# Performance work log

Measured on AMD Instinct MI355X. Metric: run time of the kernel, lower is better.

Reference implementation:

```python
import jax, jax.numpy as jnp
import numpy as np

DIM = 2048
HIDDEN = 2048
HEADS = 4
HD = HIDDEN // HEADS  # head_dim = 512
EPS = 1e-6
BATCH = 4
SEQ = 2048


def setup_inputs() -> dict:
    key = jax.random.key(0)
    k0, k1, k2, k3 = jax.random.split(key, 4)
    s = 0.02  # typical init scale; keeps exp() input gate well-behaved
    x = jax.random.normal(k0, (BATCH, SEQ, DIM), dtype=jnp.float32)
    W_in = (jax.random.normal(k1, (HIDDEN, DIM), dtype=jnp.float32) * s)
    W_gate = (jax.random.normal(k2, (4 * HIDDEN, HIDDEN), dtype=jnp.float32) * s)
    b_gate = jnp.zeros((4 * HIDDEN,), dtype=jnp.float32)
    rms_w = jnp.ones((HD,), dtype=jnp.float32)
    W_out = (jax.random.normal(k3, (DIM, HIDDEN), dtype=jnp.float32) * s)
    return {"x": x, "W_in": W_in, "W_gate": W_gate, "b_gate": b_gate,
            "rms_w": rms_w, "W_out": W_out}


def reference(x, W_in, W_gate, b_gate, rms_w, W_out):
    B, L, _ = x.shape
    # in_proj then gate_proj (the rearrange round-trip in torch is an identity
    # on the flat hidden dim, so gates come straight from x @ W_in.T)
    xp = x @ W_in.T                                    # (B, L, HIDDEN)
    gates = xp @ W_gate.T + b_gate                     # (B, L, 4*HIDDEN)
    # rearrange 'b l (h d) -> b h l d' with h=HEADS, d=4*HD
    gates = gates.reshape(B, L, HEADS, 4 * HD).transpose(0, 2, 1, 3)
    i_g, f_g, o_g, c_t = jnp.split(gates, 4, axis=-1)  # each (B, H, L, HD)
    i_g = jnp.exp(i_g)            # exponential input gate
    f_g = jax.nn.sigmoid(f_g)
    o_g = jax.nn.sigmoid(o_g)
    c_t = jnp.tanh(c_t)

    # time-major for the recurrent scan: (L, B, H, HD)
    tm = lambda a: jnp.moveaxis(a, 2, 0)

    def step(c, g):
        i, f, o, cd = g
        c = f * c + i * cd                                         # cell update
        c_norm = c * jax.lax.rsqrt(jnp.mean(c * c, axis=-1, keepdims=True) + EPS) * rms_w
        h = o * jnp.tanh(c_norm)
        return c, h

    c0 = jnp.zeros((B, HEADS, HD), dtype=x.dtype)
    _, hs = jax.lax.scan(step, c0, (tm(i_g), tm(f_g), tm(o_g), tm(c_t)))
    # (L, B, H, HD) -> (B, L, H*HD)
    h_out = jnp.moveaxis(hs, 0, 1).reshape(B, L, HIDDEN)
    return h_out @ W_out.T                             # (B, L, DIM)
```

## Files before the change

### kernel.cpp

```cpp
#include <hip/hip_runtime.h>
#include <hip/hip_bf16.h>
#include <stdint.h>

#define DIMN    2048
#define HIDDEN  2048
#define NHEADS  4
#define HDIM    512
#define BATCH   4
#define SEQ     2048
#define NTOK    (BATCH*SEQ)
#define G4      (4*HIDDEN)
#define EPSV    1e-6f
#define CHUNK   128
#define NCHUNK  (SEQ/CHUNK)

typedef short short8 __attribute__((ext_vector_type(8)));
typedef float floatx4 __attribute__((ext_vector_type(4)));

union BV8 { uint4 u; __hip_bfloat16 h[8]; unsigned short s[8]; };

__device__ __forceinline__ float fast_sigmoid(float x) {
    return 1.0f / (1.0f + __expf(-x));
}
__device__ __forceinline__ float fast_tanh(float x) {
    return 1.0f - 2.0f / (__expf(2.0f * x) + 1.0f);
}
__device__ __forceinline__ float b2f(unsigned short u) {
    union { unsigned int ui; float f; } v; v.ui = ((unsigned int)u) << 16; return v.f;
}

__device__ __forceinline__ void gld_lds16(const void* gp, void* lp) {
    __builtin_amdgcn_global_load_lds(
        (const __attribute__((address_space(1))) void*)gp,
        (__attribute__((address_space(3))) void*)lp, 16, 0, 0);
}

__global__ __launch_bounds__(256) void cast_f32_bf16(
    const float* __restrict__ in, __hip_bfloat16* __restrict__ out, int n8)
{
    int i = blockIdx.x * 256 + threadIdx.x;
    if (i >= n8) return;
    const float4* p = (const float4*)(in + (size_t)i * 8);
    float4 a = p[0], b = p[1];
    BV8 v;
    v.h[0] = __float2bfloat16(a.x); v.h[1] = __float2bfloat16(a.y);
    v.h[2] = __float2bfloat16(a.z); v.h[3] = __float2bfloat16(a.w);
    v.h[4] = __float2bfloat16(b.x); v.h[5] = __float2bfloat16(b.y);
    v.h[6] = __float2bfloat16(b.z); v.h[7] = __float2bfloat16(b.w);
    *(uint4*)(out + (size_t)i * 8) = v.u;
}

template <int EPILOGUE, int ASRC>
__global__ __launch_bounds__(512, 2) void gemm256(
    const __hip_bfloat16* __restrict__ A,
    const __hip_bfloat16* __restrict__ Bt,
    void* __restrict__ Cout,
    const float* __restrict__ bias,
    int M, int N, int K, int lda)
{
    __shared__ __align__(16) short sA[2][256 * 64];
    __shared__ __align__(16) short sB[2][256 * 64];

    const int tid  = threadIdx.x;
    const int wave = tid >> 6, lane = tid & 63;
    const int wm = wave >> 2, wn = wave & 3;
    const int quad = lane >> 4, lr = lane & 15;
    const int r8  = lane >> 3;
    const int gcs = ((lane & 7) ^ r8) * 8;
    const int rl7 = lr & 7;

    const int gx   = gridDim.x;
    const int nwg  = gx * gridDim.y;
    const int orig = blockIdx.y * gx + blockIdx.x;
    const int wg   = (orig & 7) * (nwg >> 3) + (orig >> 3);
    const int bm = wg / gx, bn = wg % gx;

    const short* Ag = (const short*)A + (size_t)(bm * 256) * lda;
    const short* Bg = (const short*)Bt + (size_t)(bn * 256) * K;

    floatx4 acc[8][4];
#pragma unroll
    for (int i = 0; i < 8; ++i)
#pragma unroll
        for (int j = 0; j < 4; ++j) acc[i][j] = (floatx4)0.0f;

    const int NT = K >> 6;

    auto stageA = [&](int kt, int qm) {
        const int kb = kt << 6;
        size_t acol;
        if (ASRC == 0) acol = (size_t)(kb + gcs);
        else           acol = (size_t)(((kb >> 9) << 11) + (kb & 511) + gcs);
        short* dst = &sA[kt & 1][0];
#pragma unroll
        for (int e = 0; e < 2; ++e) {
            const int base = qm * 128 + e * 64 + wave * 8;
            const int row  = base + r8;
            const int grow = ((row >> 6) & 1) * 128 + qm * 64 + (row & 63);
            gld_lds16(Ag + (size_t)grow * lda + acol, dst + base * 64);
        }
    };
    auto stageB = [&](int kt, int qn) {
        const int kb = kt << 6;
        short* dst = &sB[kt & 1][0];
#pragma unroll
        for (int e = 0; e < 2; ++e) {
            const int base = qn * 128 + e * 64 + wave * 8;
            const int row  = base + r8;
            const int grow = ((row >> 5) & 3) * 64 + qn * 32 + (row & 31);
            gld_lds16(Bg + (size_t)grow * K + kb + gcs, dst + base * 64);
        }
    };

    stageA(0, 0); stageB(0, 0); stageB(0, 1); stageA(0, 1);
    stageA(1, 0); stageB(1, 0); stageB(1, 1);
    asm volatile("s_waitcnt vmcnt(6)" ::: "memory");
    __builtin_amdgcn_s_barrier();

    short8 av[4][2], b0[2][2], b1[2][2];

    for (int t = 0; t < NT; ++t) {
        const short* lA = &sA[t & 1][0];
        const short* lB = &sB[t & 1][0];

#pragma unroll
        for (int kc = 0; kc < 2; ++kc) {
            const int co = (((kc * 4 + quad) ^ rl7) << 3);
#pragma unroll
            for (int m = 0; m < 4; ++m)
                av[m][kc] = *(const short8*)&lA[(wm * 64 + m * 16 + lr) * 64 + co];
#pragma unroll
            for (int j = 0; j < 2; ++j)
                b0[j][kc] = *(const short8*)&lB[(wn * 32 + j * 16 + lr) * 64 + co];
        }
        if (t + 1 < NT) stageA(t + 1, 1);
        __builtin_amdgcn_s_barrier();
        asm volatile("s_waitcnt lgkmcnt(0)" ::: "memory");
        __builtin_amdgcn_sched_barrier(0);
        __builtin_amdgcn_s_setprio(1);
#pragma unroll
        for (int m = 0; m < 4; ++m)
#pragma unroll
            for (int j = 0; j < 2; ++j)
#pragma unroll
                for (int kc = 0; kc < 2; ++kc)
                    acc[m][j] = __builtin_amdgcn_mfma_f32_16x16x32_bf16(
                        av[m][kc], b0[j][kc], acc[m][j], 0, 0, 0);
        __builtin_amdgcn_s_setprio(0);
        __builtin_amdgcn_s_barrier();

#pragma unroll
        for (int kc = 0; kc < 2; ++kc) {
            const int co = (((kc * 4 + quad) ^ rl7) << 3);
#pragma unroll
            for (int j = 0; j < 2; ++j)
                b1[j][kc] = *(const short8*)&lB[(128 + wn * 32 + j * 16 + lr) * 64 + co];
        }
        if (t + 2 < NT) stageA(t + 2, 0);
        __builtin_amdgcn_s_barrier();
        asm volatile("s_waitcnt lgkmcnt(0)" ::: "memory");
        __builtin_amdgcn_sched_barrier(0);
        __builtin_amdgcn_s_setprio(1);
#pragma unroll
        for (int m = 0; m < 4; ++m)
#pragma unroll
            for (int j = 0; j < 2; ++j)
#pragma unroll
                for (int kc = 0; kc < 2; ++kc)
                    acc[m][2 + j] = __builtin_amdgcn_mfma_f32_16x16x32_bf16(
                        av[m][kc], b1[j][kc], acc[m][2 + j], 0, 0, 0);
        __builtin_amdgcn_s_setprio(0);
        __builtin_amdgcn_s_barrier();

#pragma unroll
        for (int kc = 0; kc < 2; ++kc) {
            const int co = (((kc * 4 + quad) ^ rl7) << 3);
#pragma unroll
            for (int m = 0; m < 4; ++m)
                av[m][kc] = *(const short8*)&lA[(128 + wm * 64 + m * 16 + lr) * 64 + co];
        }
        if (t + 2 < NT) stageB(t + 2, 0);
        __builtin_amdgcn_s_barrier();
        asm volatile("s_waitcnt lgkmcnt(0)" ::: "memory");
        __builtin_amdgcn_sched_barrier(0);
        __builtin_amdgcn_s_setprio(1);
#pragma unroll
        for (int m = 0; m < 4; ++m)
#pragma unroll
            for (int j = 0; j < 2; ++j)
#pragma unroll
                for (int kc = 0; kc < 2; ++kc)
                    acc[4 + m][2 + j] = __builtin_amdgcn_mfma_f32_16x16x32_bf16(
                        av[m][kc], b1[j][kc], acc[4 + m][2 + j], 0, 0, 0);
        __builtin_amdgcn_s_setprio(0);
        __builtin_amdgcn_s_barrier();

        if (t + 2 < NT) stageB(t + 2, 1);
        __builtin_amdgcn_s_barrier();
        __builtin_amdgcn_s_setprio(1);
#pragma unroll
        for (int m = 0; m < 4; ++m)
#pragma unroll
            for (int j = 0; j < 2; ++j)
#pragma unroll
                for (int kc = 0; kc < 2; ++kc)
                    acc[4 + m][j] = __builtin_amdgcn_mfma_f32_16x16x32_bf16(
                        av[m][kc], b0[j][kc], acc[4 + m][j], 0, 0, 0);
        __builtin_amdgcn_s_setprio(0);
        if (t < NT - 2)       asm volatile("s_waitcnt vmcnt(6)" ::: "memory");
        else if (t == NT - 2) asm volatile("s_waitcnt vmcnt(0)" ::: "memory");
        __builtin_amdgcn_s_barrier();
    }

    const int colbase = bn * 256 + wn * 64;
    const int rowbase = bm * 256 + wm * 128;

    if (EPILOGUE == 0) {
        __hip_bfloat16* O = (__hip_bfloat16*)Cout;
#pragma unroll
        for (int mt = 0; mt < 8; ++mt)
#pragma unroll
            for (int nt = 0; nt < 4; ++nt)
#pragma unroll
                for (int r = 0; r < 4; ++r) {
                    int row = rowbase + mt * 16 + quad * 4 + r;
                    int col = colbase + nt * 16 + lr;
                    O[(size_t)row * N + col] = __float2bfloat16(acc[mt][nt][r]);
                }
    } else if (EPILOGUE == 1) {
        __hip_bfloat16* O = (__hip_bfloat16*)Cout;
#pragma unroll
        for (int nt = 0; nt < 4; ++nt) {
            int col = colbase + nt * 16 + lr;
            int g = (col >> 9) & 3;
            float bv = bias[col];
#pragma unroll
            for (int mt = 0; mt < 8; ++mt)
#pragma unroll
                for (int r = 0; r < 4; ++r) {
                    int row = rowbase + mt * 16 + quad * 4 + r;
                    float v = acc[mt][nt][r] + bv;
                    if (g == 0)       v = __expf(v);
                    else if (g == 3)  v = fast_tanh(v);
                    else              v = fast_sigmoid(v);
                    O[(size_t)row * N + col] = __float2bfloat16(v);
                }
        }
    } else {
        float* O = (float*)Cout;
#pragma unroll
        for (int mt = 0; mt < 8; ++mt)
#pragma unroll
            for (int nt = 0; nt < 4; ++nt)
#pragma unroll
                for (int r = 0; r < 4; ++r) {
                    int row = rowbase + mt * 16 + quad * 4 + r;
                    int col = colbase + nt * 16 + lr;
                    O[(size_t)row * N + col] = acc[mt][nt][r];
                }
    }
}

struct G16 { unsigned short i[16], f[16], c[16]; };

__device__ __forceinline__ void load_g16(const unsigned short* __restrict__ g,
                                         int t0, G16& o)
{
#pragma unroll
    for (int j = 0; j < 16; ++j) {
        const unsigned short* gp = g + (size_t)(t0 + j) * G4;
        o.i[j] = gp[0]; o.f[j] = gp[512]; o.c[j] = gp[1536];
    }
}
__device__ __forceinline__ void comp_sum16(const G16& gg, float& c, float& P)
{
#pragma unroll
    for (int j = 0; j < 16; ++j) {
        float iv = b2f(gg.i[j]);
        float fv = b2f(gg.f[j]);
        float cd = b2f(gg.c[j]);
        c = fmaf(fv, c, iv * cd);
        P *= fv;
    }
}
__device__ __forceinline__ float comp_store16(const G16& gg, float c,
                                              __hip_bfloat16* __restrict__ cb, int t0)
{
#pragma unroll
    for (int j = 0; j < 16; ++j) {
        float iv = b2f(gg.i[j]);
        float fv = b2f(gg.f[j]);
        float cd = b2f(gg.c[j]);
        c = fmaf(fv, c, iv * cd);
        cb[(size_t)(t0 + j) * HIDDEN] = __float2bfloat16(c);
    }
    return c;
}

__global__ __launch_bounds__(256) void scan_pass1(
    const __hip_bfloat16* __restrict__ gates,
    float* __restrict__ cLast, float* __restrict__ PLast)
{
    int blk = blockIdx.x;
    int dh = blk & 1;
    int j  = (blk >> 1) & 15;
    int bh = blk >> 5;
    int b = bh >> 2, h = bh & 3;
    int d = dh * 256 + threadIdx.x;
    int bhd = bh * 512 + d;

    const unsigned short* g = (const unsigned short*)gates
        + (size_t)(b * SEQ + j * CHUNK) * G4 + h * 2048 + d;

    float c = 0.0f, P = 1.0f;
    G16 A, B;
    load_g16(g, 0, A);
    for (int t0 = 0; t0 < CHUNK; t0 += 32) {
        load_g16(g, t0 + 16, B);
        comp_sum16(A, c, P);
        if (t0 + 32 < CHUNK) load_g16(g, t0 + 32, A);
        comp_sum16(B, c, P);
    }
    cLast[j * 8192 + bhd] = c;
    PLast[j * 8192 + bhd] = P;
}

__global__ __launch_bounds__(256) void scan_pass2(
    const __hip_bfloat16* __restrict__ gates,
    const float* __restrict__ cLast, const float* __restrict__ PLast,
    __hip_bfloat16* __restrict__ cbuf)
{
    int blk = blockIdx.x;
    int dh = blk & 1;
    int j  = (blk >> 1) & 15;
    int bh = blk >> 5;
    int b = bh >> 2, h = bh & 3;
    int d = dh * 256 + threadIdx.x;
    int bhd = bh * 512 + d;

    float c = 0.0f;
    for (int k = 0; k < j; ++k)
        c = fmaf(PLast[k * 8192 + bhd], c, cLast[k * 8192 + bhd]);

    const unsigned short* g = (const unsigned short*)gates
        + (size_t)(b * SEQ + j * CHUNK) * G4 + h * 2048 + d;
    __hip_bfloat16* cb = cbuf
        + (size_t)(b * SEQ + j * CHUNK) * HIDDEN + h * 512 + d;

    G16 A, B;
    load_g16(g, 0, A);
    for (int t0 = 0; t0 < CHUNK; t0 += 32) {
        load_g16(g, t0 + 16, B);
        c = comp_store16(A, c, cb, t0);
        if (t0 + 32 < CHUNK) load_g16(g, t0 + 32, A);
        c = comp_store16(B, c, cb, t0 + 16);
    }
}

__global__ __launch_bounds__(64) void norm_kernel(
    const __hip_bfloat16* __restrict__ cbuf, __hip_bfloat16* __restrict__ gates,
    const float* __restrict__ rms_w)
{
    int blk = blockIdx.x;
    int h = blk & 3;
    int t = (blk >> 2) & (SEQ - 1);
    int b = blk >> 13;
    int lane = threadIdx.x;
    size_t tok = (size_t)(b * SEQ + t);

    BV8 cv; cv.u = *(const uint4*)(cbuf + tok * HIDDEN + h * 512 + lane * 8);
    float cf[8]; float s = 0.0f;
#pragma unroll
    for (int j = 0; j < 8; ++j) { cf[j] = b2f(cv.s[j]); s += cf[j] * cf[j]; }
#pragma unroll
    for (int off = 32; off > 0; off >>= 1) s += __shfl_xor(s, off, 64);
    float rs = rsqrtf(s * (1.0f / 512.0f) + EPSV);

    BV8 ov; ov.u = *(const uint4*)(gates + tok * G4 + h * 2048 + 1024 + lane * 8);
    float4 w0 = *(const float4*)&rms_w[lane * 8];
    float4 w1 = *(const float4*)&rms_w[lane * 8 + 4];
    float w[8] = { w0.x, w0.y, w0.z, w0.w, w1.x, w1.y, w1.z, w1.w };

    BV8 hv;
#pragma unroll
    for (int j = 0; j < 8; ++j) {
        float o = b2f(ov.s[j]);
        hv.h[j] = __float2bfloat16(o * fast_tanh(cf[j] * rs * w[j]));
    }
    *(uint4*)(gates + tok * G4 + h * 2048 + lane * 8) = hv.u;
}

extern "C" void kernel_launch(void* const* d_in, const int* in_sizes, int n_in,
                              void* d_out, int out_size, void* d_ws, size_t ws_size,
                              hipStream_t stream)
{
    const float* x      = (const float*)d_in[0];
    const float* W_in   = (const float*)d_in[1];
    const float* W_gate = (const float*)d_in[2];
    const float* b_gate = (const float*)d_in[3];
    const float* rms_w  = (const float*)d_in[4];
    const float* W_out  = (const float*)d_in[5];
    float* out = (float*)d_out;

    char* base = (char*)d_ws;
    __hip_bfloat16* wgb   = (__hip_bfloat16*)base;
    __hip_bfloat16* xpb   = (__hip_bfloat16*)(base + (((size_t)32) << 20));
    __hip_bfloat16* gates = (__hip_bfloat16*)(base + (((size_t)64) << 20));
    __hip_bfloat16* wib  = gates;
    __hip_bfloat16* xb   = (__hip_bfloat16*)(base + (((size_t)72) << 20));
    __hip_bfloat16* wob  = wgb;
    float* cLast = (float*)(base + (((size_t)8) << 20));
    float* PLast = (float*)(base + (((size_t)8) << 20) + (512 << 10));
    __hip_bfloat16* cbuf = xpb;

    cast_f32_bf16<<<(HIDDEN * DIMN) / 8 / 256, 256, 0, stream>>>(W_in, wib, (HIDDEN * DIMN) / 8);
    cast_f32_bf16<<<(NTOK * DIMN) / 8 / 256, 256, 0, stream>>>(x, xb, (NTOK * DIMN) / 8);
    cast_f32_bf16<<<(G4 * HIDDEN) / 8 / 256, 256, 0, stream>>>(W_gate, wgb, (G4 * HIDDEN) / 8);

    {
        dim3 grid(HIDDEN / 256, NTOK / 256);
        gemm256<0, 0><<<grid, 512, 0, stream>>>(xb, wib, xpb, nullptr,
                                                NTOK, HIDDEN, DIMN, DIMN);
    }
    {
        dim3 grid(G4 / 256, NTOK / 256);
        gemm256<1, 0><<<grid, 512, 0, stream>>>(xpb, wgb, gates, b_gate,
                                                NTOK, G4, HIDDEN, HIDDEN);
    }
    cast_f32_bf16<<<(DIMN * HIDDEN) / 8 / 256, 256, 0, stream>>>(W_out, wob, (DIMN * HIDDEN) / 8);

    scan_pass1<<<BATCH * NHEADS * NCHUNK * 2, 256, 0, stream>>>(gates, cLast, PLast);
    scan_pass2<<<BATCH * NHEADS * NCHUNK * 2, 256, 0, stream>>>(gates, cLast, PLast, cbuf);

    norm_kernel<<<BATCH * SEQ * NHEADS, 64, 0, stream>>>(cbuf, gates, rms_w);

    {
        dim3 grid(DIMN / 256, NTOK / 256);
        gemm256<2, 1><<<grid, 512, 0, stream>>>(gates, wob, out, nullptr,
                                                NTOK, DIMN, HIDDEN, G4);
    }
}
```

Measured before the change: 654.8 us.

## Prefetch next tile's B fragments and drop per-phase barriers in GEMM loop

The GEMM main loop is restructured into a lambda unrolled by two, with ping-pong register buffers for the first B fragment set. The next tile's B fragments are loaded during the last MFMA phase of the current tile. Several s_barrier and lgkmcnt(0) waits between phases are removed, and the vmcnt wait moves earlier with a tighter count. The goal is to overlap LDS reads with MFMA work and cut synchronisation stalls. Without the explicit lgkmcnt waits, correctness depends on the compiler inserting them, and the unroll-by-two assumes NT is even.

```diff
diff --git a/kernel.cpp b/kernel.cpp
--- a/kernel.cpp
+++ b/kernel.cpp
@@ -116,12 +116,21 @@
     stageA(1, 0); stageB(1, 0); stageB(1, 1);
     asm volatile("s_waitcnt vmcnt(6)" ::: "memory");
     __builtin_amdgcn_s_barrier();
-
-    short8 av[4][2], b0[2][2], b1[2][2];
-
-    for (int t = 0; t < NT; ++t) {
-        const short* lA = &sA[t & 1][0];
-        const short* lB = &sB[t & 1][0];
+    __builtin_amdgcn_sched_barrier(0);
+
+    short8 av[4][2], b1[2][2], b0a[2][2], b0b[2][2];
+
+#pragma unroll
+    for (int kc = 0; kc < 2; ++kc) {
+        const int co = (((kc * 4 + quad) ^ rl7) << 3);
+#pragma unroll
+        for (int j = 0; j < 2; ++j)
+            b0a[j][kc] = *(const short8*)&sB[0][(wn * 32 + j * 16 + lr) * 64 + co];
+    }
+
+    auto tile_body = [&](int t_, short8 (&BCUR)[2][2], short8 (&BNEXT)[2][2]) {
+        const short* lA = &sA[t_ & 1][0];
+        const short* lB = &sB[t_ & 1][0];
 
 #pragma unroll
         for (int kc = 0; kc < 2; ++kc) {
@@ -129,14 +138,8 @@
 #pragma unroll
             for (int m = 0; m < 4; ++m)
                 av[m][kc] = *(const short8*)&lA[(wm * 64 + m * 16 + lr) * 64 + co];
-#pragma unroll
-            for (int j = 0; j < 2; ++j)
-                b0[j][kc] = *(const short8*)&lB[(wn * 32 + j * 16 + lr) * 64 + co];
-        }
-        if (t + 1 < NT) stageA(t + 1, 1);
-        __builtin_amdgcn_s_barrier();
-        asm volatile("s_waitcnt lgkmcnt(0)" ::: "memory");
-        __builtin_amdgcn_sched_barrier(0);
+        }
+        if (t_ + 1 < NT) stageA(t_ + 1, 1);
         __builtin_amdgcn_s_setprio(1);
 #pragma unroll
         for (int m = 0; m < 4; ++m)
@@ -145,9 +148,10 @@
 #pragma unroll
                 for (int kc = 0; kc < 2; ++kc)
                     acc[m][j] = __builtin_amdgcn_mfma_f32_16x16x32_bf16(
-                        av[m][kc], b0[j][kc], acc[m][j], 0, 0, 0);
+                        av[m][kc], BCUR[j][kc], acc[m][j], 0, 0, 0);
         __builtin_amdgcn_s_setprio(0);
         __builtin_amdgcn_s_barrier();
+        __builtin_amdgcn_sched_barrier(0);
 
 #pragma unroll
         for (int kc = 0; kc < 2; ++kc) {
@@ -156,10 +160,7 @@
             for (int j = 0; j < 2; ++j)
                 b1[j][kc] = *(const short8*)&lB[(128 + wn * 32 + j * 16 + lr) * 64 + co];
         }
-        if (t + 2 < NT) stageA(t + 2, 0);
-        __builtin_amdgcn_s_barrier();
-        asm volatile("s_waitcnt lgkmcnt(0)" ::: "memory");
-        __builtin_amdgcn_sched_barrier(0);
+        if (t_ + 2 < NT) stageA(t_ + 2, 0);
         __builtin_amdgcn_s_setprio(1);
 #pragma unroll
         for (int m = 0; m < 4; ++m)
@@ -171,6 +172,7 @@
                         av[m][kc], b1[j][kc], acc[m][2 + j], 0, 0, 0);
         __builtin_amdgcn_s_setprio(0);
         __builtin_amdgcn_s_barrier();
+        __builtin_amdgcn_sched_barrier(0);
 
 #pragma unroll
         for (int kc = 0; kc < 2; ++kc) {
@@ -179,10 +181,7 @@
             for (int m = 0; m < 4; ++m)
                 av[m][kc] = *(const short8*)&lA[(128 + wm * 64 + m * 16 + lr) * 64 + co];
         }
-        if (t + 2 < NT) stageB(t + 2, 0);
-        __builtin_amdgcn_s_barrier();
-        asm volatile("s_waitcnt lgkmcnt(0)" ::: "memory");
-        __builtin_amdgcn_sched_barrier(0);
+        if (t_ + 2 < NT) stageB(t_ + 2, 0);
         __builtin_amdgcn_s_setprio(1);
 #pragma unroll
         for (int m = 0; m < 4; ++m)
@@ -193,10 +192,22 @@
                     acc[4 + m][2 + j] = __builtin_amdgcn_mfma_f32_16x16x32_bf16(
                         av[m][kc], b1[j][kc], acc[4 + m][2 + j], 0, 0, 0);
         __builtin_amdgcn_s_setprio(0);
+        if (t_ < NT - 2)       asm volatile("s_waitcnt vmcnt(4)" ::: "memory");
+        else if (t_ == NT - 2) asm volatile("s_waitcnt vmcnt(0)" ::: "memory");
         __builtin_amdgcn_s_barrier();
-
-        if (t + 2 < NT) stageB(t + 2, 1);
-        __builtin_amdgcn_s_barrier();
+        __builtin_amdgcn_sched_barrier(0);
+
+        if (t_ + 1 < NT) {
+            const short* lBn = &sB[(t_ + 1) & 1][0];
+#pragma unroll
+            for (int kc = 0; kc < 2; ++kc) {
+                const int co = (((kc * 4 + quad) ^ rl7) << 3);
+#pragma unroll
+                for (int j = 0; j < 2; ++j)
+                    BNEXT[j][kc] = *(const short8*)&lBn[(wn * 32 + j * 16 + lr) * 64 + co];
+            }
+        }
+        if (t_ + 2 < NT) stageB(t_ + 2, 1);
         __builtin_amdgcn_s_setprio(1);
 #pragma unroll
         for (int m = 0; m < 4; ++m)
@@ -205,11 +216,15 @@
 #pragma unroll
                 for (int kc = 0; kc < 2; ++kc)
                     acc[4 + m][j] = __builtin_amdgcn_mfma_f32_16x16x32_bf16(
-                        av[m][kc], b0[j][kc], acc[4 + m][j], 0, 0, 0);
+                        av[m][kc], BCUR[j][kc], acc[4 + m][j], 0, 0, 0);
         __builtin_amdgcn_s_setprio(0);
-        if (t < NT - 2)       asm volatile("s_waitcnt vmcnt(6)" ::: "memory");
-        else if (t == NT - 2) asm volatile("s_waitcnt vmcnt(0)" ::: "memory");
         __builtin_amdgcn_s_barrier();
+        __builtin_amdgcn_sched_barrier(0);
+    };
+
+    for (int t = 0; t < NT; t += 2) {
+        tile_body(t,     b0a, b0b);
+        tile_body(t + 1, b0b, b0a);
     }
 
     const int colbase = bn * 256 + wn * 64;
```

Measured after the change: 861.2 us. 1.32x slower.
